# Kernel optimization log

Measured on AMD Instinct MI355X. Metric: run time of the kernel, lower is better.

Reference implementation:

```python
import jax, jax.numpy as jnp
import numpy as np

B, C, H, W = 8, 256, 128, 128
HEADS, DIM_HEAD = 4, 32
HID = HEADS * DIM_HEAD  # 128


def setup_inputs() -> dict:
    key = jax.random.key(0)
    k1, k2, k3, k4 = jax.random.split(key, 4)
    x = jax.random.normal(k1, (B, C, H, W), dtype=jnp.float32)
    # 1x1 conv weights stored as [out_ch, in_ch]
    w_qkv = jax.random.normal(k2, (3 * HID, C), dtype=jnp.float32) * (1.0 / np.sqrt(C))
    w_out = jax.random.normal(k3, (C, HID), dtype=jnp.float32) * (1.0 / np.sqrt(HID))
    b_out = jax.random.normal(k4, (C,), dtype=jnp.float32) * 0.01
    return {"x": x, "w_qkv": w_qkv, "w_out": w_out, "b_out": b_out}


def reference(x, w_qkv, w_out, b_out):
    b, c, h, w = x.shape
    n = h * w
    # 1x1 conv == channel matmul
    qkv = jnp.einsum('oc,bchw->bohw', w_qkv, x)  # [b, 3*HID, h, w]
    q, k, v = jnp.split(qkv, 3, axis=1)
    # rearrange 'b (heads d) h w -> b heads d (h w)'
    def to_heads(t):
        return t.reshape(b, HEADS, DIM_HEAD, n)
    q, k, v = to_heads(q), to_heads(k), to_heads(v)
    k = jax.nn.softmax(k, axis=-1)  # over spatial n
    # q_scale is False: q used as-is
    context = jnp.einsum('bhdn,bhen->bhde', k, v)   # [b, heads, d, e] small
    out = jnp.einsum('bhde,bhdn->bhen', context, q)  # [b, heads, e, n]
    out = out.reshape(b, HID, h, w)
    out = jnp.einsum('oc,bchw->bohw', w_out, out) + b_out[None, :, None, None]
    return out
```

## Files before the change

### kernel.cpp

```cpp
#include <hip/hip_runtime.h>
#include <stdint.h>

#define BB 8
#define CIN 256
#define NSP 16384
#define HID 128

typedef __bf16 bfrag __attribute__((ext_vector_type(8)));
typedef float  f32x4 __attribute__((ext_vector_type(4)));

__device__ __forceinline__ unsigned short f2bf(float f) {
  union { float f; unsigned int u; } v; v.f = f;
  unsigned int u = v.u;
  return (unsigned short)((u + 0x7FFFu + ((u >> 16) & 1u)) >> 16);
}
__device__ __forceinline__ float bf2f(unsigned short s) {
  union { unsigned int u; float f; } v; v.u = ((unsigned int)s) << 16;
  return v.f;
}

__global__ __launch_bounds__(256) void la_cast_w(const float* __restrict__ w,
                                                 unsigned short* __restrict__ wb, int n) {
  int i = blockIdx.x * 256 + threadIdx.x;
  if (i < n) wb[i] = f2bf(w[i]);
}

__global__ __launch_bounds__(256) void la_transpose(const float* __restrict__ x,
                                                    unsigned short* __restrict__ xT) {
  __shared__ __align__(16) float tile[64][68];
  const int n0 = blockIdx.x * 64;
  const int c0 = blockIdx.y * 64;
  const int b  = blockIdx.z;
  const int t = threadIdx.x;
  const float* xp = x + (size_t)b * CIN * NSP;
  const int nseg = (t & 15) * 4;
  const int crow = t >> 4;
#pragma unroll
  for (int i = 0; i < 4; ++i) {
    const int c = crow + i * 16;
    const float4 v = *(const float4*)(xp + (size_t)(c0 + c) * NSP + n0 + nseg);
    tile[nseg + 0][c] = v.x;
    tile[nseg + 1][c] = v.y;
    tile[nseg + 2][c] = v.z;
    tile[nseg + 3][c] = v.w;
  }
  __syncthreads();
  const int n = t >> 2;
  const int seg = (t & 3) * 16;
  unsigned short* op = xT + ((size_t)b * NSP + n0 + n) * CIN + c0 + seg;
  union { unsigned short u[16]; uint4 q[2]; } pk;
#pragma unroll
  for (int k = 0; k < 16; ++k) pk.u[k] = f2bf(tile[n][seg + k]);
  *(uint4*)(op) = pk.q[0];
  *(uint4*)(op + 8) = pk.q[1];
}

__global__ __launch_bounds__(256) void la_qkv_gemm(const unsigned short* __restrict__ wq,
                                                   const unsigned short* __restrict__ xT,
                                                   unsigned short* __restrict__ kv,
                                                   unsigned short* __restrict__ qT) {
  __shared__ __align__(16) unsigned short Wt[128][40];
  __shared__ __align__(16) unsigned short Xt[128][40];
  const int mblk = blockIdx.x;
  const int n0 = blockIdx.y * 128;
  const int b = blockIdx.z;
  const int t = threadIdx.x;
  const int lane = t & 63, wv = t >> 6;
  const int wm = (wv >> 1) * 64, wn = (wv & 1) * 64;
  const int l15 = lane & 15, q = lane >> 4;
  f32x4 acc[4][4];
#pragma unroll
  for (int i = 0; i < 4; ++i)
#pragma unroll
    for (int j = 0; j < 4; ++j) acc[i][j] = 0.0f;
  const unsigned short* wbase = wq + (size_t)mblk * 128 * CIN;
  const unsigned short* xbase = xT + ((size_t)b * NSP + n0) * CIN;
  const int r = t >> 1, hh = (t & 1) * 16;
  for (int kc = 0; kc < 8; ++kc) {
    const int ko = kc * 32 + hh;
    uint4 w0 = *(const uint4*)(wbase + (size_t)r * CIN + ko);
    uint4 w1 = *(const uint4*)(wbase + (size_t)r * CIN + ko + 8);
    uint4 x0 = *(const uint4*)(xbase + (size_t)r * CIN + ko);
    uint4 x1 = *(const uint4*)(xbase + (size_t)r * CIN + ko + 8);
    *(uint4*)&Wt[r][hh] = w0;
    *(uint4*)&Wt[r][hh + 8] = w1;
    *(uint4*)&Xt[r][hh] = x0;
    *(uint4*)&Xt[r][hh + 8] = x1;
    __syncthreads();
    bfrag a[4], bf[4];
#pragma unroll
    for (int mi = 0; mi < 4; ++mi) a[mi] = *(const bfrag*)&Wt[wm + mi * 16 + l15][q * 8];
#pragma unroll
    for (int ni = 0; ni < 4; ++ni) bf[ni] = *(const bfrag*)&Xt[wn + ni * 16 + l15][q * 8];
#pragma unroll
    for (int mi = 0; mi < 4; ++mi)
#pragma unroll
      for (int ni = 0; ni < 4; ++ni)
        acc[mi][ni] = __builtin_amdgcn_mfma_f32_16x16x32_bf16(a[mi], bf[ni], acc[mi][ni], 0, 0, 0);
    __syncthreads();
  }
  if (mblk == 0) {
    unsigned short* qb = qT + (size_t)b * NSP * HID;
#pragma unroll
    for (int mi = 0; mi < 4; ++mi) {
      const int ob = wm + mi * 16 + q * 4;
#pragma unroll
      for (int ni = 0; ni < 4; ++ni) {
        const int n = n0 + wn + ni * 16 + l15;
        ushort4 pk;
        pk.x = f2bf(acc[mi][ni][0]);
        pk.y = f2bf(acc[mi][ni][1]);
        pk.z = f2bf(acc[mi][ni][2]);
        pk.w = f2bf(acc[mi][ni][3]);
        *(ushort4*)(qb + (size_t)n * HID + ob) = pk;
      }
    }
  } else {
    unsigned short* kb = kv + ((size_t)b * 256 + (size_t)(mblk - 1) * 128) * NSP;
#pragma unroll
    for (int mi = 0; mi < 4; ++mi) {
      const int ob = wm + mi * 16 + q * 4;
#pragma unroll
      for (int ni = 0; ni < 4; ++ni) {
        const int n = n0 + wn + ni * 16 + l15;
#pragma unroll
        for (int rg = 0; rg < 4; ++rg)
          kb[(size_t)(ob + rg) * NSP + n] = f2bf(acc[mi][ni][rg]);
      }
    }
  }
}

__global__ __launch_bounds__(256) void la_stats(const unsigned short* __restrict__ kv,
                                                float* __restrict__ mx, float* __restrict__ rs) {
  const int row = blockIdx.x;
  const int b = row >> 7, j = row & 127;
  const unsigned short* kr = kv + ((size_t)b * 256 + j) * NSP;
  const int t = threadIdx.x;
  float m = -3.0e38f;
  for (int i = t * 8; i < NSP; i += 2048) {
    ushort4 v0 = *(const ushort4*)(kr + i);
    ushort4 v1 = *(const ushort4*)(kr + i + 4);
    m = fmaxf(m, fmaxf(fmaxf(fmaxf(bf2f(v0.x), bf2f(v0.y)), fmaxf(bf2f(v0.z), bf2f(v0.w))),
                       fmaxf(fmaxf(bf2f(v1.x), bf2f(v1.y)), fmaxf(bf2f(v1.z), bf2f(v1.w)))));
  }
#pragma unroll
  for (int off = 32; off > 0; off >>= 1) m = fmaxf(m, __shfl_down(m, off));
  __shared__ float sm[4];
  __shared__ float bm;
  if ((t & 63) == 0) sm[t >> 6] = m;
  __syncthreads();
  if (t == 0) bm = fmaxf(fmaxf(sm[0], sm[1]), fmaxf(sm[2], sm[3]));
  __syncthreads();
  const float M = bm;
  float s = 0.f;
  for (int i = t * 8; i < NSP; i += 2048) {
    ushort4 v0 = *(const ushort4*)(kr + i);
    ushort4 v1 = *(const ushort4*)(kr + i + 4);
    s += __expf(bf2f(v0.x) - M) + __expf(bf2f(v0.y) - M) + __expf(bf2f(v0.z) - M) +
         __expf(bf2f(v0.w) - M) + __expf(bf2f(v1.x) - M) + __expf(bf2f(v1.y) - M) +
         __expf(bf2f(v1.z) - M) + __expf(bf2f(v1.w) - M);
  }
#pragma unroll
  for (int off = 32; off > 0; off >>= 1) s += __shfl_down(s, off);
  __shared__ float ss[4];
  if ((t & 63) == 0) ss[t >> 6] = s;
  __syncthreads();
  if (t == 0) {
    mx[row] = M;
    rs[row] = 1.0f / (ss[0] + ss[1] + ss[2] + ss[3]);
  }
}

__global__ __launch_bounds__(256) void la_context(const unsigned short* __restrict__ kv,
                                                  const float* __restrict__ mx,
                                                  float* __restrict__ ctxu) {
  const int bh = blockIdx.x;
  const int chunk = blockIdx.y;
  const int b = bh >> 2, h = bh & 3;
  const int t = threadIdx.x, lane = t & 63, wv = t >> 6;
  const int l15 = lane & 15, q = lane >> 4;
  const unsigned short* kbase = kv + ((size_t)b * 256 + h * 32) * NSP;
  const unsigned short* vbase = kv + ((size_t)b * 256 + 128 + h * 32) * NSP;
  const float md[2] = {mx[bh * 32 + l15], mx[bh * 32 + 16 + l15]};
  f32x4 acc[2][2];
  acc[0][0] = 0.f; acc[0][1] = 0.f; acc[1][0] = 0.f; acc[1][1] = 0.f;
  for (int it = 0; it < 8; ++it) {
    const int noff = chunk * 1024 + (it * 4 + wv) * 32 + q * 8;
    bfrag af[2], vf[2];
#pragma unroll
    for (int di = 0; di < 2; ++di) {
      const unsigned short* kr = kbase + (size_t)(di * 16 + l15) * NSP + noff;
      ushort4 v0 = *(const ushort4*)kr;
      ushort4 v1 = *(const ushort4*)(kr + 4);
      union { unsigned short u[8]; bfrag v; } pk;
      pk.u[0] = f2bf(__expf(bf2f(v0.x) - md[di]));
      pk.u[1] = f2bf(__expf(bf2f(v0.y) - md[di]));
      pk.u[2] = f2bf(__expf(bf2f(v0.z) - md[di]));
      pk.u[3] = f2bf(__expf(bf2f(v0.w) - md[di]));
      pk.u[4] = f2bf(__expf(bf2f(v1.x) - md[di]));
      pk.u[5] = f2bf(__expf(bf2f(v1.y) - md[di]));
      pk.u[6] = f2bf(__expf(bf2f(v1.z) - md[di]));
      pk.u[7] = f2bf(__expf(bf2f(v1.w) - md[di]));
      af[di] = pk.v;
    }
#pragma unroll
    for (int ei = 0; ei < 2; ++ei)
      vf[ei] = *(const bfrag*)(vbase + (size_t)(ei * 16 + l15) * NSP + noff);
#pragma unroll
    for (int di = 0; di < 2; ++di)
#pragma unroll
      for (int ei = 0; ei < 2; ++ei)
        acc[di][ei] = __builtin_amdgcn_mfma_f32_16x16x32_bf16(af[di], vf[ei], acc[di][ei], 0, 0, 0);
  }
  __shared__ float part[4][1024];
#pragma unroll
  for (int di = 0; di < 2; ++di)
#pragma unroll
    for (int ei = 0; ei < 2; ++ei)
#pragma unroll
      for (int rg = 0; rg < 4; ++rg)
        part[wv][(di * 16 + q * 4 + rg) * 32 + ei * 16 + l15] = acc[di][ei][rg];
  __syncthreads();
  float* cb = ctxu + (size_t)bh * 1024;
  for (int idx = t; idx < 1024; idx += 256)
    atomicAdd(&cb[idx], part[0][idx] + part[1][idx] + part[2][idx] + part[3][idx]);
}

__global__ __launch_bounds__(128) void la_weff(const float* __restrict__ w_out,
                                               const float* __restrict__ ctxu,
                                               const float* __restrict__ rs,
                                               unsigned short* __restrict__ weff) {
  const int o = blockIdx.x;
  const int b = blockIdx.y;
  const int cp = threadIdx.x;
  const int h = cp >> 5, d = cp & 31;
  const float* wrow = w_out + (size_t)o * HID + h * 32;
  const float* crow = ctxu + ((size_t)(b * 4 + h) * 32 + d) * 32;
  float s = 0.f;
#pragma unroll 8
  for (int e = 0; e < 32; ++e) s += wrow[e] * crow[e];
  s *= rs[(b * 4 + h) * 32 + d];
  weff[((size_t)b * 256 + o) * HID + cp] = f2bf(s);
}

__global__ __launch_bounds__(256) void la_out_gemm(const unsigned short* __restrict__ weff,
                                                   const unsigned short* __restrict__ qT,
                                                   const float* __restrict__ b_out,
                                                   float* __restrict__ out) {
  __shared__ __align__(16) unsigned short At[128][40];
  __shared__ __align__(16) unsigned short Bt[128][40];
  const int mblk = blockIdx.x;
  const int n0 = blockIdx.y * 128;
  const int b = blockIdx.z;
  const int t = threadIdx.x;
  const int lane = t & 63, wv = t >> 6;
  const int wm = (wv >> 1) * 64, wn = (wv & 1) * 64;
  const int l15 = lane & 15, q = lane >> 4;
  f32x4 acc[4][4];
#pragma unroll
  for (int i = 0; i < 4; ++i)
#pragma unroll
    for (int j = 0; j < 4; ++j) acc[i][j] = 0.0f;
  const unsigned short* abase = weff + ((size_t)b * 256 + mblk * 128) * HID;
  const unsigned short* bbase = qT + ((size_t)b * NSP + n0) * HID;
  const int r = t >> 1, hh = (t & 1) * 16;
  for (int kc = 0; kc < 4; ++kc) {
    const int ko = kc * 32 + hh;
    uint4 a0 = *(const uint4*)(abase + (size_t)r * HID + ko);
    uint4 a1 = *(const uint4*)(abase + (size_t)r * HID + ko + 8);
    uint4 b0 = *(const uint4*)(bbase + (size_t)r * HID + ko);
    uint4 b1 = *(const uint4*)(bbase + (size_t)r * HID + ko + 8);
    *(uint4*)&At[r][hh] = a0;
    *(uint4*)&At[r][hh + 8] = a1;
    *(uint4*)&Bt[r][hh] = b0;
    *(uint4*)&Bt[r][hh + 8] = b1;
    __syncthreads();
    bfrag a[4], bf[4];
#pragma unroll
    for (int mi = 0; mi < 4; ++mi) a[mi] = *(const bfrag*)&At[wm + mi * 16 + l15][q * 8];
#pragma unroll
    for (int ni = 0; ni < 4; ++ni) bf[ni] = *(const bfrag*)&Bt[wn + ni * 16 + l15][q * 8];
#pragma unroll
    for (int mi = 0; mi < 4; ++mi)
#pragma unroll
      for (int ni = 0; ni < 4; ++ni)
        acc[mi][ni] = __builtin_amdgcn_mfma_f32_16x16x32_bf16(a[mi], bf[ni], acc[mi][ni], 0, 0, 0);
    __syncthreads();
  }
  float* obase = out + ((size_t)b * 256 + mblk * 128) * NSP;
#pragma unroll
  for (int mi = 0; mi < 4; ++mi) {
    const int ob = wm + mi * 16 + q * 4;
    const float4 bias = *(const float4*)(b_out + mblk * 128 + ob);
    float ba[4] = {bias.x, bias.y, bias.z, bias.w};
#pragma unroll
    for (int ni = 0; ni < 4; ++ni) {
      const int n = n0 + wn + ni * 16 + l15;
#pragma unroll
      for (int rg = 0; rg < 4; ++rg)
        obase[(size_t)(ob + rg) * NSP + n] = acc[mi][ni][rg] + ba[rg];
    }
  }
}


extern "C" void kernel_launch(void* const* d_in, const int* in_sizes, int n_in,
                              void* d_out, int out_size, void* d_ws, size_t ws_size,
                              hipStream_t stream) {
  (void)in_sizes; (void)n_in; (void)out_size; (void)ws_size;
  const float* x     = (const float*)d_in[0];
  const float* w_qkv = (const float*)d_in[1];
  const float* w_out = (const float*)d_in[2];
  const float* b_out = (const float*)d_in[3];
  float* out = (float*)d_out;
  char* ws = (char*)d_ws;
  unsigned short* xT  = (unsigned short*)(ws);
  unsigned short* kv  = (unsigned short*)(ws + 67108864);
  unsigned short* qT  = (unsigned short*)(ws + 134217728);
  float* mx           = (float*)(ws + 167772160);
  float* rs           = (float*)(ws + 167776256);
  float* ctxu         = (float*)(ws + 167780352);
  unsigned short* weff = (unsigned short*)(ws + 167911424);
  unsigned short* wqb  = (unsigned short*)(ws + 168435712);

  hipMemsetAsync(ctxu, 0, 131072, stream);
  la_cast_w<<<dim3(384), dim3(256), 0, stream>>>(w_qkv, wqb, 384 * 256);
  la_transpose<<<dim3(NSP / 64, CIN / 64, BB), dim3(256), 0, stream>>>(x, xT);
  la_qkv_gemm<<<dim3(3, NSP / 128, BB), dim3(256), 0, stream>>>(wqb, xT, kv, qT);
  la_stats<<<dim3(BB * 128), dim3(256), 0, stream>>>(kv, mx, rs);
  la_context<<<dim3(32, 16), dim3(256), 0, stream>>>(kv, mx, ctxu);
  la_weff<<<dim3(256, BB), dim3(128), 0, stream>>>(w_out, ctxu, rs, weff);
  la_out_gemm<<<dim3(2, NSP / 128, BB), dim3(256), 0, stream>>>(weff, qT, b_out, out);
}
```

Baseline: 354.0 us.

## Fuse K/V projection with softmax exp and context accumulation per spatial chunk

Splits the QKV GEMM into a Q-only GEMM and a fused kernel that computes K and V for a 128-position chunk. The fused kernel applies exp to K, accumulates the per-row softmax denominators with atomics, and computes the partial context in shared memory. Partial contexts go to a per-chunk buffer, and a small kernel reduces them. This removes the full K/V tensor being written to and reread from global memory, and drops the separate stats kernel. In exchange, softmax no longer subtracts the row max, so exp can overflow when K values are large, and the kernel's larger shared-memory and register footprint limits occupancy.

```diff
diff --git a/kernel.cpp b/kernel.cpp
--- a/kernel.cpp
+++ b/kernel.cpp
@@ -55,15 +55,13 @@
   *(uint4*)(op + 8) = pk.q[1];
 }
 
-__global__ __launch_bounds__(256) void la_qkv_gemm(const unsigned short* __restrict__ wq,
-                                                   const unsigned short* __restrict__ xT,
-                                                   unsigned short* __restrict__ kv,
-                                                   unsigned short* __restrict__ qT) {
+__global__ __launch_bounds__(256) void la_q_gemm(const unsigned short* __restrict__ wq,
+                                                 const unsigned short* __restrict__ xT,
+                                                 unsigned short* __restrict__ qT) {
   __shared__ __align__(16) unsigned short Wt[128][40];
   __shared__ __align__(16) unsigned short Xt[128][40];
-  const int mblk = blockIdx.x;
-  const int n0 = blockIdx.y * 128;
-  const int b = blockIdx.z;
+  const int n0 = blockIdx.x * 128;
+  const int b = blockIdx.y;
   const int t = threadIdx.x;
   const int lane = t & 63, wv = t >> 6;
   const int wm = (wv >> 1) * 64, wn = (wv & 1) * 64;
@@ -73,7 +71,7 @@
   for (int i = 0; i < 4; ++i)
 #pragma unroll
     for (int j = 0; j < 4; ++j) acc[i][j] = 0.0f;
-  const unsigned short* wbase = wq + (size_t)mblk * 128 * CIN;
+  const unsigned short* wbase = wq;
   const unsigned short* xbase = xT + ((size_t)b * NSP + n0) * CIN;
   const int r = t >> 1, hh = (t & 1) * 16;
   for (int kc = 0; kc < 8; ++kc) {
@@ -99,137 +97,144 @@
         acc[mi][ni] = __builtin_amdgcn_mfma_f32_16x16x32_bf16(a[mi], bf[ni], acc[mi][ni], 0, 0, 0);
     __syncthreads();
   }
-  if (mblk == 0) {
-    unsigned short* qb = qT + (size_t)b * NSP * HID;
-#pragma unroll
-    for (int mi = 0; mi < 4; ++mi) {
-      const int ob = wm + mi * 16 + q * 4;
-#pragma unroll
-      for (int ni = 0; ni < 4; ++ni) {
-        const int n = n0 + wn + ni * 16 + l15;
-        ushort4 pk;
-        pk.x = f2bf(acc[mi][ni][0]);
-        pk.y = f2bf(acc[mi][ni][1]);
-        pk.z = f2bf(acc[mi][ni][2]);
-        pk.w = f2bf(acc[mi][ni][3]);
-        *(ushort4*)(qb + (size_t)n * HID + ob) = pk;
+  unsigned short* qb = qT + (size_t)b * NSP * HID;
+#pragma unroll
+  for (int mi = 0; mi < 4; ++mi) {
+    const int ob = wm + mi * 16 + q * 4;
+#pragma unroll
+    for (int ni = 0; ni < 4; ++ni) {
+      const int n = n0 + wn + ni * 16 + l15;
+      ushort4 pk;
+      pk.x = f2bf(acc[mi][ni][0]);
+      pk.y = f2bf(acc[mi][ni][1]);
+      pk.z = f2bf(acc[mi][ni][2]);
+      pk.w = f2bf(acc[mi][ni][3]);
+      *(ushort4*)(qb + (size_t)n * HID + ob) = pk;
+    }
+  }
+}
+
+__global__ __launch_bounds__(256, 2) void la_kv_ctx(const unsigned short* __restrict__ wq,
+                                                    const unsigned short* __restrict__ xT,
+                                                    float* __restrict__ ctxp,
+                                                    float* __restrict__ sums) {
+  __shared__ union {
+    struct { unsigned short Wt[256][40]; unsigned short Xt[128][40]; } g;
+    struct { unsigned short Lk[128][136]; unsigned short Lv[128][136]; } e;
+  } sh;
+  const int chunk = blockIdx.x;
+  const int n0 = chunk * 128;
+  const int b = blockIdx.y;
+  const int t = threadIdx.x;
+  const int lane = t & 63, wv = t >> 6;
+  const int l15 = lane & 15, q = lane >> 4;
+  const int wm = wv * 64;
+  f32x4 acc[4][8];
+#pragma unroll
+  for (int i = 0; i < 4; ++i)
+#pragma unroll
+    for (int j = 0; j < 8; ++j) acc[i][j] = 0.0f;
+  const unsigned short* wbase = wq + 128 * CIN;
+  const unsigned short* xbase = xT + ((size_t)b * NSP + n0) * CIN;
+  const int xr = t >> 1, xh = (t & 1) * 16;
+  for (int kc = 0; kc < 8; ++kc) {
+    const int ko = kc * 32;
+    uint4 w0 = *(const uint4*)(wbase + (size_t)t * CIN + ko);
+    uint4 w1 = *(const uint4*)(wbase + (size_t)t * CIN + ko + 8);
+    uint4 w2 = *(const uint4*)(wbase + (size_t)t * CIN + ko + 16);
+    uint4 w3 = *(const uint4*)(wbase + (size_t)t * CIN + ko + 24);
+    uint4 x0 = *(const uint4*)(xbase + (size_t)xr * CIN + ko + xh);
+    uint4 x1 = *(const uint4*)(xbase + (size_t)xr * CIN + ko + xh + 8);
+    *(uint4*)&sh.g.Wt[t][0]  = w0;
+    *(uint4*)&sh.g.Wt[t][8]  = w1;
+    *(uint4*)&sh.g.Wt[t][16] = w2;
+    *(uint4*)&sh.g.Wt[t][24] = w3;
+    *(uint4*)&sh.g.Xt[xr][xh]     = x0;
+    *(uint4*)&sh.g.Xt[xr][xh + 8] = x1;
+    __syncthreads();
+    bfrag a[4], bb[8];
+#pragma unroll
+    for (int mi = 0; mi < 4; ++mi) a[mi] = *(const bfrag*)&sh.g.Wt[wm + mi * 16 + l15][q * 8];
+#pragma unroll
+    for (int ni = 0; ni < 8; ++ni) bb[ni] = *(const bfrag*)&sh.g.Xt[ni * 16 + l15][q * 8];
+#pragma unroll
+    for (int mi = 0; mi < 4; ++mi)
+#pragma unroll
+      for (int ni = 0; ni < 8; ++ni)
+        acc[mi][ni] = __builtin_amdgcn_mfma_f32_16x16x32_bf16(a[mi], bb[ni], acc[mi][ni], 0, 0, 0);
+    __syncthreads();
+  }
+  const int isV = wv >> 1;
+  const int rb = (wv & 1) * 64;
+  unsigned short (*Lp)[136] = isV ? sh.e.Lv : sh.e.Lk;
+  float sp[16];
+#pragma unroll
+  for (int i = 0; i < 16; ++i) sp[i] = 0.f;
+#pragma unroll
+  for (int mi = 0; mi < 4; ++mi)
+#pragma unroll
+    for (int ni = 0; ni < 8; ++ni)
+#pragma unroll
+      for (int rg = 0; rg < 4; ++rg) {
+        float val = acc[mi][ni][rg];
+        if (!isV) { val = __expf(val); sp[mi * 4 + rg] += val; }
+        Lp[rb + mi * 16 + q * 4 + rg][ni * 16 + l15] = f2bf(val);
       }
+  if (!isV) {
+#pragma unroll
+    for (int i = 0; i < 16; ++i) {
+      float s = sp[i];
+      s += __shfl_down(s, 8, 16);
+      s += __shfl_down(s, 4, 16);
+      s += __shfl_down(s, 2, 16);
+      s += __shfl_down(s, 1, 16);
+      if (l15 == 0)
+        atomicAdd(&sums[b * 128 + rb + (i >> 2) * 16 + q * 4 + (i & 3)], s);
     }
-  } else {
-    unsigned short* kb = kv + ((size_t)b * 256 + (size_t)(mblk - 1) * 128) * NSP;
-#pragma unroll
-    for (int mi = 0; mi < 4; ++mi) {
-      const int ob = wm + mi * 16 + q * 4;
-#pragma unroll
-      for (int ni = 0; ni < 4; ++ni) {
-        const int n = n0 + wn + ni * 16 + l15;
-#pragma unroll
-        for (int rg = 0; rg < 4; ++rg)
-          kb[(size_t)(ob + rg) * NSP + n] = f2bf(acc[mi][ni][rg]);
-      }
-    }
-  }
-}
-
-__global__ __launch_bounds__(256) void la_stats(const unsigned short* __restrict__ kv,
-                                                float* __restrict__ mx, float* __restrict__ rs) {
-  const int row = blockIdx.x;
-  const int b = row >> 7, j = row & 127;
-  const unsigned short* kr = kv + ((size_t)b * 256 + j) * NSP;
-  const int t = threadIdx.x;
-  float m = -3.0e38f;
-  for (int i = t * 8; i < NSP; i += 2048) {
-    ushort4 v0 = *(const ushort4*)(kr + i);
-    ushort4 v1 = *(const ushort4*)(kr + i + 4);
-    m = fmaxf(m, fmaxf(fmaxf(fmaxf(bf2f(v0.x), bf2f(v0.y)), fmaxf(bf2f(v0.z), bf2f(v0.w))),
-                       fmaxf(fmaxf(bf2f(v1.x), bf2f(v1.y)), fmaxf(bf2f(v1.z), bf2f(v1.w)))));
-  }
-#pragma unroll
-  for (int off = 32; off > 0; off >>= 1) m = fmaxf(m, __shfl_down(m, off));
-  __shared__ float sm[4];
-  __shared__ float bm;
-  if ((t & 63) == 0) sm[t >> 6] = m;
+  }
   __syncthreads();
-  if (t == 0) bm = fmaxf(fmaxf(sm[0], sm[1]), fmaxf(sm[2], sm[3]));
-  __syncthreads();
-  const float M = bm;
+  const int h = wv;
+  f32x4 c2[2][2];
+  c2[0][0] = 0.f; c2[0][1] = 0.f; c2[1][0] = 0.f; c2[1][1] = 0.f;
+#pragma unroll
+  for (int nit = 0; nit < 4; ++nit) {
+    bfrag ka[2], vb2[2];
+#pragma unroll
+    for (int d2 = 0; d2 < 2; ++d2)
+      ka[d2] = *(const bfrag*)&sh.e.Lk[h * 32 + d2 * 16 + l15][nit * 32 + q * 8];
+#pragma unroll
+    for (int e2 = 0; e2 < 2; ++e2)
+      vb2[e2] = *(const bfrag*)&sh.e.Lv[h * 32 + e2 * 16 + l15][nit * 32 + q * 8];
+#pragma unroll
+    for (int d2 = 0; d2 < 2; ++d2)
+#pragma unroll
+      for (int e2 = 0; e2 < 2; ++e2)
+        c2[d2][e2] = __builtin_amdgcn_mfma_f32_16x16x32_bf16(ka[d2], vb2[e2], c2[d2][e2], 0, 0, 0);
+  }
+  float* cp = ctxp + ((size_t)chunk * 32 + b * 4 + h) * 1024;
+#pragma unroll
+  for (int d2 = 0; d2 < 2; ++d2)
+#pragma unroll
+    for (int e2 = 0; e2 < 2; ++e2)
+#pragma unroll
+      for (int rg = 0; rg < 4; ++rg)
+        cp[(d2 * 16 + q * 4 + rg) * 32 + e2 * 16 + l15] = c2[d2][e2][rg];
+}
+
+__global__ __launch_bounds__(256) void la_reduce(const float* __restrict__ ctxp,
+                                                 float* __restrict__ ctxu) {
+  const int gid = blockIdx.x * 256 + threadIdx.x;
+  const int g = blockIdx.y;
+  const float* p = ctxp + (size_t)g * 32 * 32768 + gid;
   float s = 0.f;
-  for (int i = t * 8; i < NSP; i += 2048) {
-    ushort4 v0 = *(const ushort4*)(kr + i);
-    ushort4 v1 = *(const ushort4*)(kr + i + 4);
-    s += __expf(bf2f(v0.x) - M) + __expf(bf2f(v0.y) - M) + __expf(bf2f(v0.z) - M) +
-         __expf(bf2f(v0.w) - M) + __expf(bf2f(v1.x) - M) + __expf(bf2f(v1.y) - M) +
-         __expf(bf2f(v1.z) - M) + __expf(bf2f(v1.w) - M);
-  }
-#pragma unroll
-  for (int off = 32; off > 0; off >>= 1) s += __shfl_down(s, off);
-  __shared__ float ss[4];
-  if ((t & 63) == 0) ss[t >> 6] = s;
-  __syncthreads();
-  if (t == 0) {
-    mx[row] = M;
-    rs[row] = 1.0f / (ss[0] + ss[1] + ss[2] + ss[3]);
-  }
-}
-
-__global__ __launch_bounds__(256) void la_context(const unsigned short* __restrict__ kv,
-                                                  const float* __restrict__ mx,
-                                                  float* __restrict__ ctxu) {
-  const int bh = blockIdx.x;
-  const int chunk = blockIdx.y;
-  const int b = bh >> 2, h = bh & 3;
-  const int t = threadIdx.x, lane = t & 63, wv = t >> 6;
-  const int l15 = lane & 15, q = lane >> 4;
-  const unsigned short* kbase = kv + ((size_t)b * 256 + h * 32) * NSP;
-  const unsigned short* vbase = kv + ((size_t)b * 256 + 128 + h * 32) * NSP;
-  const float md[2] = {mx[bh * 32 + l15], mx[bh * 32 + 16 + l15]};
-  f32x4 acc[2][2];
-  acc[0][0] = 0.f; acc[0][1] = 0.f; acc[1][0] = 0.f; acc[1][1] = 0.f;
-  for (int it = 0; it < 8; ++it) {
-    const int noff = chunk * 1024 + (it * 4 + wv) * 32 + q * 8;
-    bfrag af[2], vf[2];
-#pragma unroll
-    for (int di = 0; di < 2; ++di) {
-      const unsigned short* kr = kbase + (size_t)(di * 16 + l15) * NSP + noff;
-      ushort4 v0 = *(const ushort4*)kr;
-      ushort4 v1 = *(const ushort4*)(kr + 4);
-      union { unsigned short u[8]; bfrag v; } pk;
-      pk.u[0] = f2bf(__expf(bf2f(v0.x) - md[di]));
-      pk.u[1] = f2bf(__expf(bf2f(v0.y) - md[di]));
-      pk.u[2] = f2bf(__expf(bf2f(v0.z) - md[di]));
-      pk.u[3] = f2bf(__expf(bf2f(v0.w) - md[di]));
-      pk.u[4] = f2bf(__expf(bf2f(v1.x) - md[di]));
-      pk.u[5] = f2bf(__expf(bf2f(v1.y) - md[di]));
-      pk.u[6] = f2bf(__expf(bf2f(v1.z) - md[di]));
-      pk.u[7] = f2bf(__expf(bf2f(v1.w) - md[di]));
-      af[di] = pk.v;
-    }
-#pragma unroll
-    for (int ei = 0; ei < 2; ++ei)
-      vf[ei] = *(const bfrag*)(vbase + (size_t)(ei * 16 + l15) * NSP + noff);
-#pragma unroll
-    for (int di = 0; di < 2; ++di)
-#pragma unroll
-      for (int ei = 0; ei < 2; ++ei)
-        acc[di][ei] = __builtin_amdgcn_mfma_f32_16x16x32_bf16(af[di], vf[ei], acc[di][ei], 0, 0, 0);
-  }
-  __shared__ float part[4][1024];
-#pragma unroll
-  for (int di = 0; di < 2; ++di)
-#pragma unroll
-    for (int ei = 0; ei < 2; ++ei)
-#pragma unroll
-      for (int rg = 0; rg < 4; ++rg)
-        part[wv][(di * 16 + q * 4 + rg) * 32 + ei * 16 + l15] = acc[di][ei][rg];
-  __syncthreads();
-  float* cb = ctxu + (size_t)bh * 1024;
-  for (int idx = t; idx < 1024; idx += 256)
-    atomicAdd(&cb[idx], part[0][idx] + part[1][idx] + part[2][idx] + part[3][idx]);
+#pragma unroll
+  for (int c = 0; c < 32; ++c) s += p[(size_t)c * 32768];
+  atomicAdd(&ctxu[gid], s);
 }
 
 __global__ __launch_bounds__(128) void la_weff(const float* __restrict__ w_out,
                                                const float* __restrict__ ctxu,
-                                               const float* __restrict__ rs,
+                                               const float* __restrict__ sums,
                                                unsigned short* __restrict__ weff) {
   const int o = blockIdx.x;
   const int b = blockIdx.y;
@@ -240,7 +245,7 @@
   float s = 0.f;
 #pragma unroll 8
   for (int e = 0; e < 32; ++e) s += wrow[e] * crow[e];
-  s *= rs[(b * 4 + h) * 32 + d];
+  s *= (1.0f / sums[b * 128 + h * 32 + d]);
   weff[((size_t)b * 256 + o) * HID + cp] = f2bf(s);
 }
 
@@ -315,21 +320,20 @@
   const float* b_out = (const float*)d_in[3];
   float* out = (float*)d_out;
   char* ws = (char*)d_ws;
-  unsigned short* xT  = (unsigned short*)(ws);
-  unsigned short* kv  = (unsigned short*)(ws + 67108864);
-  unsigned short* qT  = (unsigned short*)(ws + 134217728);
-  float* mx           = (float*)(ws + 167772160);
-  float* rs           = (float*)(ws + 167776256);
-  float* ctxu         = (float*)(ws + 167780352);
-  unsigned short* weff = (unsigned short*)(ws + 167911424);
-  unsigned short* wqb  = (unsigned short*)(ws + 168435712);
-
-  hipMemsetAsync(ctxu, 0, 131072, stream);
+  unsigned short* xT   = (unsigned short*)(ws);
+  unsigned short* qT   = (unsigned short*)(ws + 67108864);
+  float* ctxp          = (float*)(ws + 100663296);
+  float* ctxu          = (float*)(ws + 117440512);
+  float* sums          = (float*)(ws + 117571584);
+  unsigned short* weff = (unsigned short*)(ws + 117575680);
+  unsigned short* wqb  = (unsigned short*)(ws + 118099968);
+
+  hipMemsetAsync(ctxu, 0, 131072 + 4096, stream);
   la_cast_w<<<dim3(384), dim3(256), 0, stream>>>(w_qkv, wqb, 384 * 256);
   la_transpose<<<dim3(NSP / 64, CIN / 64, BB), dim3(256), 0, stream>>>(x, xT);
-  la_qkv_gemm<<<dim3(3, NSP / 128, BB), dim3(256), 0, stream>>>(wqb, xT, kv, qT);
-  la_stats<<<dim3(BB * 128), dim3(256), 0, stream>>>(kv, mx, rs);
-  la_context<<<dim3(32, 16), dim3(256), 0, stream>>>(kv, mx, ctxu);
-  la_weff<<<dim3(256, BB), dim3(128), 0, stream>>>(w_out, ctxu, rs, weff);
+  la_q_gemm<<<dim3(NSP / 128, BB), dim3(256), 0, stream>>>(wqb, xT, qT);
+  la_kv_ctx<<<dim3(NSP / 128, BB), dim3(256), 0, stream>>>(wqb, xT, ctxp, sums);
+  la_reduce<<<dim3(128, 4), dim3(256), 0, stream>>>(ctxp, ctxu);
+  la_weff<<<dim3(256, BB), dim3(128), 0, stream>>>(w_out, ctxu, sums, weff);
   la_out_gemm<<<dim3(2, NSP / 128, BB), dim3(256), 0, stream>>>(weff, qT, b_out, out);
 }
```

Measured after the change: 353.5 us. Within noise of the previous version (-0.1%).
